# Optimization experiments

Measured on AMD Instinct MI355X. Metric: run time of the kernel, lower is better.

## Reference

```python
import jax, jax.numpy as jnp
import numpy as np

B = 32
N_INPUTS = 16384
N_DET = 65536
K = 32  # max_inputs_per_detector


def setup_inputs() -> dict:
    key = jax.random.key(0)
    k1, k2 = jax.random.split(key)
    x = jax.random.normal(k1, (B, N_INPUTS), dtype=jnp.float32)
    # detector membership table: each detector watches K input neuron ids
    detectors = jax.random.randint(k2, (N_DET, K), 0, N_INPUTS, dtype=jnp.int32)
    return {"x": x, "detectors": detectors}


def reference(x, detectors):
    """Winner-take-all inhibition.

    For each batch row and each detector, the member input with the largest
    activation is the winner; every other (valid, id != -1) member is
    inhibited (its winning_stat is incremented). Output spikes (1.0) only for
    inputs never inhibited by any detector (winning_stat == 0), matching
    spiking_inhibition=True where the output is a pure binary mask.
    """
    Bn, n_inputs = x.shape
    D, Kd = detectors.shape
    valid = detectors >= 0                      # [D, K] (-1 = padding)
    safe_idx = jnp.where(valid, detectors, 0)   # [D, K]
    neg_inf = jnp.float32(-jnp.inf)
    col = jnp.arange(Kd, dtype=jnp.int32)[None, :]

    def per_batch(xb):  # xb: [n_inputs]
        vals = jnp.where(valid, xb[safe_idx], neg_inf)     # [D, K] gather
        widx = jnp.argmax(vals, axis=-1)                   # winner slot per detector
        loser = valid & (col != widx[:, None])             # inhibited members
        stat = jnp.zeros((n_inputs,), jnp.int32).at[safe_idx.reshape(-1)].add(
            loser.reshape(-1).astype(jnp.int32))           # scatter-add counts
        return stat

    stat = jax.vmap(per_batch)(x)               # [B, n_inputs]
    out = (stat == 0).astype(jnp.float32)       # spike iff never inhibited
    return out
```

## Files before the change

### kernel.cpp

```cpp
#include <hip/hip_runtime.h>

#define N_INPUTS 16384
#define N_DET    65536
#define KD       32
#define BATCH    32
#define SLICES   16
#define DPB      (N_DET / SLICES)
#define THREADS  1024

__device__ __forceinline__ float max3f(float a, float b, float c) {
    return fmaxf(fmaxf(a, b), c);
}

__device__ __forceinline__ unsigned compact_even(unsigned v) {
    v &= 0x55555555u;
    v = (v | (v >> 1)) & 0x33333333u;
    v = (v | (v >> 2)) & 0x0F0F0F0Fu;
    v = (v | (v >> 4)) & 0x00FF00FFu;
    v = (v | (v >> 8)) & 0x0000FFFFu;
    return v;
}

__global__ __launch_bounds__(THREADS) void inhibit(const float* __restrict__ x,
                                                   const int* __restrict__ det,
                                                   unsigned long long* __restrict__ pm) {
    __shared__ float2   xs[N_INPUTS];
    __shared__ unsigned fl[N_INPUTS / 16];

    const int slice = blockIdx.x;
    const int pair  = blockIdx.y;
    const int tid   = threadIdx.x;

    fl[tid] = 0u;

    const float4* x0 = (const float4*)(x + (size_t)(2 * pair) * N_INPUTS);
    const float4* x1 = (const float4*)(x + (size_t)(2 * pair + 1) * N_INPUTS);
    float4* xs4 = (float4*)xs;
#pragma unroll
    for (int k = 0; k < N_INPUTS / 4 / THREADS; ++k) {
        int t = tid + k * THREADS;
        float4 a = x0[t], b = x1[t];
        xs4[2 * t + 0] = make_float4(a.x, b.x, a.y, b.y);
        xs4[2 * t + 1] = make_float4(a.z, b.z, a.w, b.w);
    }
    __syncthreads();

    const int4* det4 = (const int4*)det;
#pragma unroll 1
    for (int j = 0; j < DPB / THREADS; ++j) {
        const int   d    = slice * DPB + j * THREADS + tid;
        const int4* drow = det4 + (size_t)d * 8;
        int ids[KD];
#pragma unroll
        for (int q = 0; q < 8; ++q) {
            int4 r = drow[q];
            ids[q * 4 + 0] = r.x; ids[q * 4 + 1] = r.y;
            ids[q * 4 + 2] = r.z; ids[q * 4 + 3] = r.w;
        }

        float2 v[KD];
#pragma unroll
        for (int s = 0; s < KD; ++s) v[s] = xs[ids[s]];

        float t0[11], t1[11];
#pragma unroll
        for (int i = 0; i < 10; ++i) {
            t0[i] = max3f(v[3 * i].x, v[3 * i + 1].x, v[3 * i + 2].x);
            t1[i] = max3f(v[3 * i].y, v[3 * i + 1].y, v[3 * i + 2].y);
        }
        t0[10] = fmaxf(v[30].x, v[31].x);
        t1[10] = fmaxf(v[30].y, v[31].y);
        float m0 = fmaxf(max3f(max3f(t0[0], t0[1], t0[2]),
                               max3f(t0[3], t0[4], t0[5]),
                               max3f(t0[6], t0[7], t0[8])),
                         fmaxf(t0[9], t0[10]));
        float m1 = fmaxf(max3f(max3f(t1[0], t1[1], t1[2]),
                               max3f(t1[3], t1[4], t1[5]),
                               max3f(t1[6], t1[7], t1[8])),
                         fmaxf(t1[9], t1[10]));

        int s0 = 0, s1 = 0;
#pragma unroll
        for (int s = KD - 1; s >= 0; --s) {
            s0 = (v[s].x == m0) ? s : s0;
            s1 = (v[s].y == m1) ? s : s1;
        }

        const unsigned wm0 = 1u << s0, wm1 = 1u << s1;
#pragma unroll
        for (int s = 0; s < KD; ++s) {
            int id = ids[s];
            unsigned lose = 3u ^ (((wm0 >> s) & 1u) | (((wm1 >> s) & 1u) << 1));
            atomicOr(&fl[id >> 4], lose << ((id & 15) * 2));
        }
    }
    __syncthreads();

    unsigned f  = fl[tid];
    unsigned b0 = compact_even(f);
    unsigned b1 = compact_even(f >> 1);
    unsigned short* pm0 =
        (unsigned short*)(pm + ((size_t)(2 * pair) * SLICES + slice) * (N_INPUTS / 64));
    unsigned short* pm1 =
        (unsigned short*)(pm + ((size_t)(2 * pair + 1) * SLICES + slice) * (N_INPUTS / 64));
    pm0[tid] = (unsigned short)b0;
    pm1[tid] = (unsigned short)b1;
}

__global__ __launch_bounds__(256) void finalize(const unsigned* __restrict__ pm,
                                                float* __restrict__ out) {
    const int gid = blockIdx.x * 256 + threadIdx.x;
    const int b   = gid >> 14;
    const int i   = gid & (N_INPUTS - 1);
    unsigned acc = 0;
#pragma unroll
    for (int s = 0; s < SLICES; ++s)
        acc |= pm[((b * SLICES + s) << 9) + (i >> 5)];
    out[gid] = ((acc >> (i & 31)) & 1u) ? 0.0f : 1.0f;
}

extern "C" void kernel_launch(void* const* d_in, const int* in_sizes, int n_in,
                              void* d_out, int out_size, void* d_ws, size_t ws_size,
                              hipStream_t stream) {
    const float* x   = (const float*)d_in[0];
    const int*   det = (const int*)d_in[1];
    unsigned long long* pm = (unsigned long long*)d_ws;

    dim3 grid(SLICES, BATCH / 2);
    inhibit<<<grid, THREADS, 0, stream>>>(x, det, pm);
    finalize<<<BATCH * N_INPUTS / 256, 256, 0, stream>>>((const unsigned*)pm,
                                                         (float*)d_out);
}
```

Before: 86.26 us.

## Pack activations to bf16 pairs in LDS with exact tie resolution from global

The LDS copy of the two batch rows is reduced to the upper 16 bits of each float, packed into one 32-bit word per input, which halves shared memory to 64KB so more blocks fit per CU. Argmax is taken on the truncated values; when several slots tie at the truncated maximum, the winner is re-resolved by reading the full-precision floats from global memory. Slices are doubled to 32 for more parallelism, detector ids are packed into 16-bit pairs to save registers, and the finalize kernel now writes 32 outputs per thread as float4 stores. The cost is extra global reads whenever truncation creates ties, plus more partial masks to OR together in finalize.

```diff
diff --git a/kernel.cpp b/kernel.cpp
--- a/kernel.cpp
+++ b/kernel.cpp
@@ -4,7 +4,7 @@
 #define N_DET    65536
 #define KD       32
 #define BATCH    32
-#define SLICES   16
+#define SLICES   32
 #define DPB      (N_DET / SLICES)
 #define THREADS  1024
 
@@ -21,10 +21,25 @@
     return v;
 }
 
-__global__ __launch_bounds__(THREADS) void inhibit(const float* __restrict__ x,
-                                                   const int* __restrict__ det,
-                                                   unsigned long long* __restrict__ pm) {
-    __shared__ float2   xs[N_INPUTS];
+__device__ __forceinline__ int resolve32(unsigned c, const unsigned pk[16],
+                                         const float* __restrict__ xb) {
+    float best = -INFINITY;
+    int   win  = 0;
+#pragma unroll
+    for (int s = 0; s < KD; ++s) {
+        if ((c >> s) & 1u) {
+            unsigned id = (pk[s >> 1] >> ((s & 1) * 16)) & 0xFFFFu;
+            float    xf = xb[id];
+            if (xf > best) { best = xf; win = s; }
+        }
+    }
+    return win;
+}
+
+__global__ __launch_bounds__(THREADS, 8) void inhibit(const float* __restrict__ x,
+                                                      const int* __restrict__ det,
+                                                      unsigned* __restrict__ pm) {
+    __shared__ unsigned xs[N_INPUTS];
     __shared__ unsigned fl[N_INPUTS / 16];
 
     const int slice = blockIdx.x;
@@ -33,15 +48,22 @@
 
     fl[tid] = 0u;
 
-    const float4* x0 = (const float4*)(x + (size_t)(2 * pair) * N_INPUTS);
-    const float4* x1 = (const float4*)(x + (size_t)(2 * pair + 1) * N_INPUTS);
-    float4* xs4 = (float4*)xs;
+    const float* __restrict__ xb0 = x + (size_t)(2 * pair) * N_INPUTS;
+    const float* __restrict__ xb1 = x + (size_t)(2 * pair + 1) * N_INPUTS;
+
+    const uint4* a4 = (const uint4*)xb0;
+    const uint4* b4 = (const uint4*)xb1;
+    uint4* xs4 = (uint4*)xs;
 #pragma unroll
     for (int k = 0; k < N_INPUTS / 4 / THREADS; ++k) {
         int t = tid + k * THREADS;
-        float4 a = x0[t], b = x1[t];
-        xs4[2 * t + 0] = make_float4(a.x, b.x, a.y, b.y);
-        xs4[2 * t + 1] = make_float4(a.z, b.z, a.w, b.w);
+        uint4 a = a4[t], b = b4[t];
+        uint4 w;
+        w.x = (a.x >> 16) | (b.x & 0xFFFF0000u);
+        w.y = (a.y >> 16) | (b.y & 0xFFFF0000u);
+        w.z = (a.z >> 16) | (b.z & 0xFFFF0000u);
+        w.w = (a.w >> 16) | (b.w & 0xFFFF0000u);
+        xs4[t] = w;
     }
     __syncthreads();
 
@@ -50,48 +72,64 @@
     for (int j = 0; j < DPB / THREADS; ++j) {
         const int   d    = slice * DPB + j * THREADS + tid;
         const int4* drow = det4 + (size_t)d * 8;
-        int ids[KD];
+
+        unsigned pk[16];
+        float    m0 = 0.f, m1 = 0.f;
+        unsigned e0 = 0u,  e1 = 0u;
 #pragma unroll
-        for (int q = 0; q < 8; ++q) {
-            int4 r = drow[q];
-            ids[q * 4 + 0] = r.x; ids[q * 4 + 1] = r.y;
-            ids[q * 4 + 2] = r.z; ids[q * 4 + 3] = r.w;
+        for (int h = 0; h < 2; ++h) {
+            int4 r0 = drow[4 * h + 0], r1 = drow[4 * h + 1];
+            int4 r2 = drow[4 * h + 2], r3 = drow[4 * h + 3];
+            int ids[16] = { r0.x, r0.y, r0.z, r0.w, r1.x, r1.y, r1.z, r1.w,
+                            r2.x, r2.y, r2.z, r2.w, r3.x, r3.y, r3.z, r3.w };
+            unsigned w[16];
+#pragma unroll
+            for (int s = 0; s < 16; ++s) w[s] = xs[ids[s]];
+#pragma unroll
+            for (int p = 0; p < 8; ++p)
+                pk[h * 8 + p] = (unsigned)ids[2 * p] | ((unsigned)ids[2 * p + 1] << 16);
+
+            float v0[16], v1[16];
+#pragma unroll
+            for (int s = 0; s < 16; ++s) {
+                v0[s] = __uint_as_float(w[s] << 16);
+                v1[s] = __uint_as_float(w[s] & 0xFFFF0000u);
+            }
+            float t0 = max3f(v0[0], v0[1], v0[2]),  t1 = max3f(v0[3], v0[4], v0[5]);
+            float t2 = max3f(v0[6], v0[7], v0[8]),  t3 = max3f(v0[9], v0[10], v0[11]);
+            float t4 = max3f(v0[12], v0[13], v0[14]);
+            float mh0 = fmaxf(max3f(t0, t1, t2), max3f(t3, t4, v0[15]));
+            float u0 = max3f(v1[0], v1[1], v1[2]),  u1 = max3f(v1[3], v1[4], v1[5]);
+            float u2 = max3f(v1[6], v1[7], v1[8]),  u3 = max3f(v1[9], v1[10], v1[11]);
+            float u4 = max3f(v1[12], v1[13], v1[14]);
+            float mh1 = fmaxf(max3f(u0, u1, u2), max3f(u3, u4, v1[15]));
+
+            unsigned f0 = 0u, f1 = 0u;
+#pragma unroll
+            for (int s = 0; s < 16; ++s) {
+                f0 |= (v0[s] == mh0) ? (1u << s) : 0u;
+                f1 |= (v1[s] == mh1) ? (1u << s) : 0u;
+            }
+            if (h == 0) { m0 = mh0; e0 = f0; m1 = mh1; e1 = f1; }
+            else {
+                e0 = (m0 >= mh0 ? e0 : 0u) | (mh0 >= m0 ? (f0 << 16) : 0u);
+                e1 = (m1 >= mh1 ? e1 : 0u) | (mh1 >= m1 ? (f1 << 16) : 0u);
+                m0 = fmaxf(m0, mh0);
+                m1 = fmaxf(m1, mh1);
+            }
         }
-
-        float2 v[KD];
-#pragma unroll
-        for (int s = 0; s < KD; ++s) v[s] = xs[ids[s]];
-
-        float t0[11], t1[11];
-#pragma unroll
-        for (int i = 0; i < 10; ++i) {
-            t0[i] = max3f(v[3 * i].x, v[3 * i + 1].x, v[3 * i + 2].x);
-            t1[i] = max3f(v[3 * i].y, v[3 * i + 1].y, v[3 * i + 2].y);
-        }
-        t0[10] = fmaxf(v[30].x, v[31].x);
-        t1[10] = fmaxf(v[30].y, v[31].y);
-        float m0 = fmaxf(max3f(max3f(t0[0], t0[1], t0[2]),
-                               max3f(t0[3], t0[4], t0[5]),
-                               max3f(t0[6], t0[7], t0[8])),
-                         fmaxf(t0[9], t0[10]));
-        float m1 = fmaxf(max3f(max3f(t1[0], t1[1], t1[2]),
-                               max3f(t1[3], t1[4], t1[5]),
-                               max3f(t1[6], t1[7], t1[8])),
-                         fmaxf(t1[9], t1[10]));
-
-        int s0 = 0, s1 = 0;
-#pragma unroll
-        for (int s = KD - 1; s >= 0; --s) {
-            s0 = (v[s].x == m0) ? s : s0;
-            s1 = (v[s].y == m1) ? s : s1;
-        }
+        int s0, s1;
+        if (e0 & (e0 - 1)) s0 = resolve32(e0, pk, xb0);
+        else               s0 = __builtin_ctz(e0);
+        if (e1 & (e1 - 1)) s1 = resolve32(e1, pk, xb1);
+        else               s1 = __builtin_ctz(e1);
 
         const unsigned wm0 = 1u << s0, wm1 = 1u << s1;
 #pragma unroll
         for (int s = 0; s < KD; ++s) {
-            int id = ids[s];
+            unsigned id   = (pk[s >> 1] >> ((s & 1) * 16)) & 0xFFFFu;
             unsigned lose = 3u ^ (((wm0 >> s) & 1u) | (((wm1 >> s) & 1u) << 1));
-            atomicOr(&fl[id >> 4], lose << ((id & 15) * 2));
+            atomicOr(&fl[id >> 4], lose << ((id & 15u) * 2u));
         }
     }
     __syncthreads();
@@ -100,9 +138,9 @@
     unsigned b0 = compact_even(f);
     unsigned b1 = compact_even(f >> 1);
     unsigned short* pm0 =
-        (unsigned short*)(pm + ((size_t)(2 * pair) * SLICES + slice) * (N_INPUTS / 64));
+        (unsigned short*)(pm + ((size_t)(2 * pair) * SLICES + slice) * (N_INPUTS / 32));
     unsigned short* pm1 =
-        (unsigned short*)(pm + ((size_t)(2 * pair + 1) * SLICES + slice) * (N_INPUTS / 64));
+        (unsigned short*)(pm + ((size_t)(2 * pair + 1) * SLICES + slice) * (N_INPUTS / 32));
     pm0[tid] = (unsigned short)b0;
     pm1[tid] = (unsigned short)b1;
 }
@@ -110,13 +148,22 @@
 __global__ __launch_bounds__(256) void finalize(const unsigned* __restrict__ pm,
                                                 float* __restrict__ out) {
     const int gid = blockIdx.x * 256 + threadIdx.x;
-    const int b   = gid >> 14;
-    const int i   = gid & (N_INPUTS - 1);
+    const int b   = gid >> 9;
+    const int w   = gid & 511;
     unsigned acc = 0;
 #pragma unroll
     for (int s = 0; s < SLICES; ++s)
-        acc |= pm[((b * SLICES + s) << 9) + (i >> 5)];
-    out[gid] = ((acc >> (i & 31)) & 1u) ? 0.0f : 1.0f;
+        acc |= pm[((b * SLICES + s) << 9) + w];
+    float4* o4 = (float4*)(out + ((size_t)gid << 5));
+#pragma unroll
+    for (int q = 0; q < 8; ++q) {
+        float4 r;
+        r.x = ((acc >> (4 * q + 0)) & 1u) ? 0.0f : 1.0f;
+        r.y = ((acc >> (4 * q + 1)) & 1u) ? 0.0f : 1.0f;
+        r.z = ((acc >> (4 * q + 2)) & 1u) ? 0.0f : 1.0f;
+        r.w = ((acc >> (4 * q + 3)) & 1u) ? 0.0f : 1.0f;
+        o4[q] = r;
+    }
 }
 
 extern "C" void kernel_launch(void* const* d_in, const int* in_sizes, int n_in,
@@ -124,10 +171,9 @@
                               hipStream_t stream) {
     const float* x   = (const float*)d_in[0];
     const int*   det = (const int*)d_in[1];
-    unsigned long long* pm = (unsigned long long*)d_ws;
+    unsigned*    pm  = (unsigned*)d_ws;
 
     dim3 grid(SLICES, BATCH / 2);
     inhibit<<<grid, THREADS, 0, stream>>>(x, det, pm);
-    finalize<<<BATCH * N_INPUTS / 256, 256, 0, stream>>>((const unsigned*)pm,
-                                                         (float*)d_out);
+    finalize<<<BATCH * (N_INPUTS / 32) / 256, 256, 0, stream>>>(pm, (float*)d_out);
 }
```

Result: slower. 154.6 us (+79.2%).
